# Kernel tuning notes

Hardware: AMD Instinct MI355X
Metric: run time of the kernel (lower is better)

The kernel has to match this reference:

```python
import jax, jax.numpy as jnp
import numpy as np

T, B, D = 64, 256, 2000
TN, E, H, A, V = 3000, 256, 256, 128, 128
PS, PE, S = 64, 64, 128
G1N, G1L, G2N, G2L = 1500, 4, 1500, 6


def setup_inputs():
    key = jax.random.key(0)
    ks = jax.random.split(key, 32)
    def nrm(k, shape, s=0.05):
        return jax.random.normal(k, shape, dtype=jnp.float32) * s
    inp = {}
    inp["X"] = jax.random.uniform(ks[0], (T, B, D), dtype=jnp.float32)
    inp["profiles"] = nrm(ks[1], (B, PS), 1.0)
    inp["ini_embd"] = nrm(ks[2], (TN, E), 1.0)
    inp["Wa_w"] = nrm(ks[3], (2 * E, A))
    inp["Wa_b"] = jnp.zeros((A,), jnp.float32)
    inp["Ua_w"] = nrm(ks[4], (A, 1))
    inp["gru_Wih"] = nrm(ks[5], (3 * H, E))
    inp["gru_Whh"] = nrm(ks[6], (3 * H, H))
    inp["gru_bih"] = jnp.zeros((3 * H,), jnp.float32)
    inp["gru_bhh"] = jnp.zeros((3 * H,), jnp.float32)
    inp["tranH_w"] = nrm(ks[7], (H + PE, E))
    inp["tranH_b"] = jnp.zeros((E,), jnp.float32)
    inp["out_w"] = nrm(ks[8], (H + V + PE, D))
    inp["out_b"] = jnp.zeros((D,), jnp.float32)
    inp["erase_w"] = nrm(ks[9], (E, V))
    inp["erase_b"] = jnp.zeros((V,), jnp.float32)
    inp["add_w"] = nrm(ks[10], (E, V))
    inp["add_b"] = jnp.zeros((V,), jnp.float32)
    inp["iniVam"] = nrm(ks[11], (S, V), 1.0)
    inp["emP_w"] = nrm(ks[12], (PS, PE))
    inp["emP_b"] = jnp.zeros((PE,), jnp.float32)
    inp["attnP_w"] = nrm(ks[13], (PE + V, PE))
    inp["attnP_b"] = jnp.zeros((PE,), jnp.float32)
    inp["KMIds"] = jax.random.randint(ks[14], (S,), 0, TN, dtype=jnp.int32)
    inp["leaves1"] = jax.random.randint(ks[15], (G1N, G1L), 0, TN, dtype=jnp.int32)
    inp["anc1"] = jax.random.randint(ks[16], (G1N, G1L), 0, TN, dtype=jnp.int32)
    inp["leaves2"] = jax.random.randint(ks[17], (G2N, G2L), 0, TN, dtype=jnp.int32)
    inp["anc2"] = jax.random.randint(ks[18], (G2N, G2L), 0, TN, dtype=jnp.int32)
    inp["mapInfo"] = jax.random.randint(ks[19], (D,), 0, G1N + G2N, dtype=jnp.int32)
    lens = jnp.sort(jax.random.randint(ks[20], (B,), 1, T + 1, dtype=jnp.int32))[::-1]
    inp["X_lengths"] = lens.at[0].set(T)
    return inp


def _forward(floats, ints):
    (X, profiles, ini_embd, Wa_w, Wa_b, Ua_w, gru_Wih, gru_Whh, gru_bih, gru_bhh,
     tranH_w, tranH_b, out_w, out_b, erase_w, erase_b, add_w, add_b, iniVam,
     emP_w, emP_b, attnP_w, attnP_b) = floats
    KMIds, leaves1, anc1, leaves2, anc2, mapInfo, X_lengths = ints

    # GRAM-style ontology attention over (leaf, ancestor) pairs, grouped by path length
    def group_embed(leaves, anc):
        le = ini_embd[leaves]                                     # [N,L,E]
        ae = ini_embd[anc]                                        # [N,L,E]
        hdn = jnp.tanh(jnp.concatenate([le, ae], axis=2) @ Wa_w + Wa_b)
        w = jax.nn.softmax(hdn @ Ua_w, axis=1)                    # [N,L,1]
        return jnp.sum(w * ae, axis=1)                            # [N,E]

    embedMat = jnp.concatenate([group_embed(leaves1, anc1),
                                group_embed(leaves2, anc2)], axis=0)[mapInfo]  # [D,E]
    Xe = jnp.einsum('tbd,de->tbe', X, embedMat)                   # [T,B,E]

    # packed-sequence GRU: frozen state / zero output beyond each sample's length
    mask = (jnp.arange(T)[:, None] < X_lengths[None, :])[..., None]  # [T,B,1]

    def gru_step(h, tup):
        x_t, m_t = tup
        gx = x_t @ gru_Wih.T + gru_bih
        gh = h @ gru_Whh.T + gru_bhh
        r = jax.nn.sigmoid(gx[:, :H] + gh[:, :H])
        z = jax.nn.sigmoid(gx[:, H:2 * H] + gh[:, H:2 * H])
        n = jnp.tanh(gx[:, 2 * H:] + r * gh[:, 2 * H:])
        h_new = (1.0 - z) * n + z * h
        h = jnp.where(m_t, h_new, h)
        return h, jnp.where(m_t, h, 0.0)

    h0 = jnp.zeros((B, H), jnp.float32)
    _, gru_out = jax.lax.scan(gru_step, h0, (Xe, mask))           # [T,B,H]

    prof = profiles @ emP_w + emP_b                               # [B,PE]
    prof_rep = jnp.broadcast_to(prof[None], (T, B, PE))
    tran = jnp.concatenate([gru_out, prof_rep], axis=2) @ tranH_w + tranH_b  # [T,B,E]
    KM = ini_embd[KMIds]                                          # [S,E]
    slot_w = jax.nn.softmax(jnp.einsum('tbe,se->tbs', tran, KM), axis=2)     # [T,B,S]

    # erase/add gates depend only on Xe -> precompute, then scan VM recurrence
    erase = jax.nn.sigmoid(Xe @ erase_w + erase_b)                # [T,B,V]
    add = jnp.tanh(Xe @ add_w + add_b)                            # [T,B,V]

    def mem_step(VM, tup):
        sw, er, ad = tup                                          # [B,S],[B,V],[B,V]
        read = jnp.einsum('bs,bsv->bv', sw, VM)
        VM = VM * (1.0 - sw[:, :, None] * er[:, None, :]) + sw[:, :, None] * ad[:, None, :]
        return VM, read

    VM0 = jnp.broadcast_to(iniVam[None], (B, S, V))
    _, read = jax.lax.scan(mem_step, VM0, (slot_w, erase, add))   # read: [T,B,V]

    attn = jax.nn.relu(jnp.concatenate([prof_rep, read], axis=2) @ attnP_w + attnP_b)
    prof2 = prof_rep * attn
    final = jnp.concatenate([gru_out, read, prof2], axis=2)       # [T,B,H+V+PE]
    # dropout is identity (eval / drop_rate=0)
    return jax.nn.softmax(final @ out_w + out_b, axis=2)          # [T,B,D]


def reference(X, profiles, ini_embd, Wa_w, Wa_b, Ua_w, gru_Wih, gru_Whh, gru_bih, gru_bhh, tranH_w, tranH_b, out_w, out_b, erase_w, erase_b, add_w, add_b, iniVam, emP_w, emP_b, attnP_w, attnP_b, KMIds, leaves1, anc1, leaves2, anc2, mapInfo, X_lengths):
    floats = (X, profiles, ini_embd, Wa_w, Wa_b, Ua_w, gru_Wih, gru_Whh, gru_bih, gru_bhh,
              tranH_w, tranH_b, out_w, out_b, erase_w, erase_b, add_w, add_b, iniVam,
              emP_w, emP_b, attnP_w, attnP_b)
    ints = (KMIds, leaves1, anc1, leaves2, anc2, mapInfo, X_lengths)
    return _forward(floats, ints)
```

## Files before the change

### kernel.cpp

```cpp
#include <hip/hip_runtime.h>
#include <hip/hip_bf16.h>
#include <cmath>

#define T_  64
#define B_  256
#define D_  2000
#define TN_ 3000
#define E_  256
#define H_  256
#define A_  128
#define V_  128
#define PS_ 64
#define PE_ 64
#define S_  128
#define G1N_ 1500
#define G1L_ 4
#define G2N_ 1500
#define G2L_ 6
#define M_  (T_ * B_)
#define KF_ (H_ + V_ + PE_)
#define NREG 28

typedef __attribute__((ext_vector_type(8))) short short8_t;
typedef __attribute__((ext_vector_type(4))) float floatx4;
typedef _Float16 __attribute__((ext_vector_type(2))) h2_t;
typedef _Float16 __attribute__((ext_vector_type(8))) h8_t;

static __device__ __forceinline__ float sigmoidf_(float x) {
    return 1.0f / (1.0f + __expf(-x));
}

static __device__ __forceinline__ void bsplit_(float v, __hip_bfloat16& hi, __hip_bfloat16& lo) {
    hi = __float2bfloat16(v);
    lo = __float2bfloat16(v - __bfloat162float(hi));
}

static __device__ __forceinline__ float dot2_(unsigned int w, unsigned int h, float acc) {
    union { unsigned int u; h2_t h; } cw, ch;
    cw.u = w; ch.u = h;
#if __has_builtin(__builtin_amdgcn_fdot2)
    return __builtin_amdgcn_fdot2(cw.h, ch.h, acc, false);
#else
    return acc + (float)cw.h[0] * (float)ch.h[0] + (float)cw.h[1] * (float)ch.h[1];
#endif
}

template<int DT>
static __device__ __forceinline__ floatx4 mfma16_(short8_t a, short8_t b, floatx4 c) {
    if constexpr (DT == 0) {
        return __builtin_amdgcn_mfma_f32_16x16x32_bf16(a, b, c, 0, 0, 0);
    } else {
        union { short8_t s; h8_t h; } ua, ub;
        ua.s = a; ub.s = b;
        return __builtin_amdgcn_mfma_f32_16x16x32_f16(ua.h, ub.h, c, 0, 0, 0);
    }
}

template<int EPI, bool ACCUM, int OUTMODE, int NPH, int DT>
__global__ __launch_bounds__(256)
void k_mgemm3(const __hip_bfloat16* __restrict__ Ahi, const __hip_bfloat16* __restrict__ Alo,
              const __hip_bfloat16* __restrict__ Bhi, const __hip_bfloat16* __restrict__ Blo,
              const float* __restrict__ bias, float* __restrict__ Cf,
              __hip_bfloat16* __restrict__ Chi, __hip_bfloat16* __restrict__ Clo,
              int K, int Nreal, int nblk)
{
    __shared__ __align__(16) short As[4096];
    __shared__ __align__(16) short Bs[4096];

    const int tid  = threadIdx.x;
    const int lane = tid & 63;
    const int w    = tid >> 6;
    const int wm   = w >> 1, wn = w & 1;
    const int lr   = lane & 15;
    const int lkc  = lane >> 4;

    const int bx = blockIdx.x;
    const int m0 = (bx / nblk) * 128;
    const int n0 = (bx % nblk) * 128;

    const int fa = 2 * w;
    const size_t aoff0 = (size_t)(m0 + fa * 16 + lr) * K + lkc * 8;
    const size_t aoff1 = aoff0 + (size_t)16 * K;
    const size_t boff0 = (size_t)(n0 + fa * 16 + lr) * K + lkc * 8;
    const size_t boff1 = boff0 + (size_t)16 * K;

    floatx4 acc[4][4];
#pragma unroll
    for (int i = 0; i < 4; ++i)
#pragma unroll
        for (int j = 0; j < 4; ++j) acc[i][j] = floatx4{0.f, 0.f, 0.f, 0.f};

#pragma unroll 1
    for (int ph = 0; ph < NPH; ++ph) {
        const __hip_bfloat16* Ap = (ph == 2) ? Alo : Ahi;
        const __hip_bfloat16* Bp = (ph == 1) ? Blo : Bhi;

        short8_t ra0 = *(const short8_t*)(const void*)(Ap + aoff0);
        short8_t ra1 = *(const short8_t*)(const void*)(Ap + aoff1);
        short8_t rb0 = *(const short8_t*)(const void*)(Bp + boff0);
        short8_t rb1 = *(const short8_t*)(const void*)(Bp + boff1);

        for (int k0 = 0; k0 < K; k0 += 32) {
            __syncthreads();
            *(short8_t*)(void*)&As[(fa    ) * 512 + lane * 8] = ra0;
            *(short8_t*)(void*)&As[(fa + 1) * 512 + lane * 8] = ra1;
            *(short8_t*)(void*)&Bs[(fa    ) * 512 + lane * 8] = rb0;
            *(short8_t*)(void*)&Bs[(fa + 1) * 512 + lane * 8] = rb1;
            __syncthreads();

            if (k0 + 32 < K) {
                int kn = k0 + 32;
                ra0 = *(const short8_t*)(const void*)(Ap + aoff0 + kn);
                ra1 = *(const short8_t*)(const void*)(Ap + aoff1 + kn);
                rb0 = *(const short8_t*)(const void*)(Bp + boff0 + kn);
                rb1 = *(const short8_t*)(const void*)(Bp + boff1 + kn);
            }

            short8_t af[4], bf[4];
#pragma unroll
            for (int i = 0; i < 4; ++i)
                af[i] = *(const short8_t*)(const void*)&As[(wm * 4 + i) * 512 + lane * 8];
#pragma unroll
            for (int j = 0; j < 4; ++j)
                bf[j] = *(const short8_t*)(const void*)&Bs[(wn * 4 + j) * 512 + lane * 8];
#pragma unroll
            for (int i = 0; i < 4; ++i)
#pragma unroll
                for (int j = 0; j < 4; ++j)
                    acc[i][j] = mfma16_<DT>(af[i], bf[j], acc[i][j]);
        }
    }

#pragma unroll
    for (int i = 0; i < 4; ++i) {
        const int row = m0 + wm * 64 + i * 16 + (lane >> 4) * 4;
#pragma unroll
        for (int j = 0; j < 4; ++j) {
            const int col = n0 + wn * 64 + j * 16 + (lane & 15);
            if (col < Nreal) {
                float bv = bias ? bias[col] : 0.0f;
#pragma unroll
                for (int r = 0; r < 4; ++r) {
                    float v = acc[i][j][r] + bv;
                    if (EPI == 1) v = (col < 128) ? sigmoidf_(v) : tanhf(v);
                    size_t o = (size_t)(row + r) * Nreal + col;
                    if (OUTMODE == 0) {
                        if (ACCUM) v += Cf[o];
                        Cf[o] = v;
                    } else {
                        __hip_bfloat16 h, l;
                        bsplit_(v, h, l);
                        Chi[o] = h; Clo[o] = l;
                    }
                }
            }
        }
    }
}

__global__ __launch_bounds__(256)
void k_mgemmX(const float* __restrict__ A,
              const __hip_bfloat16* __restrict__ Bhi, const __hip_bfloat16* __restrict__ Blo,
              __hip_bfloat16* __restrict__ Chi, __hip_bfloat16* __restrict__ Clo)
{
    const int KP = 2048, KR = 2000, NN = 256, nblk = 2;
    __shared__ __align__(16) short Ah[4096];
    __shared__ __align__(16) short Al[4096];
    __shared__ __align__(16) short Bh[4096];
    __shared__ __align__(16) short Bl[4096];

    const int tid  = threadIdx.x;
    const int lane = tid & 63;
    const int w    = tid >> 6;
    const int wm   = w >> 1, wn = w & 1;
    const int lr   = lane & 15;
    const int lkc  = lane >> 4;

    const int bx = blockIdx.x;
    const int m0 = (bx / nblk) * 128;
    const int n0 = (bx % nblk) * 128;

    const int fa = 2 * w;
    const float* arow0 = A + (size_t)(m0 + fa * 16 + lr) * KR;
    const float* arow1 = arow0 + (size_t)16 * KR;
    const size_t boff0 = (size_t)(n0 + fa * 16 + lr) * KP + lkc * 8;
    const size_t boff1 = boff0 + (size_t)16 * KP;

    floatx4 acc[4][4];
#pragma unroll
    for (int i = 0; i < 4; ++i)
#pragma unroll
        for (int j = 0; j < 4; ++j) acc[i][j] = floatx4{0.f, 0.f, 0.f, 0.f};

    float a0v[8], a1v[8];
    short8_t bh0, bh1, bl0, bl1;

#define LOADA8(ROW, KB, DST)                                                  \
    if ((KB) + 7 < KR) {                                                      \
        float4 p_ = *(const float4*)((ROW) + (KB));                           \
        float4 q_ = *(const float4*)((ROW) + (KB) + 4);                       \
        DST[0]=p_.x; DST[1]=p_.y; DST[2]=p_.z; DST[3]=p_.w;                   \
        DST[4]=q_.x; DST[5]=q_.y; DST[6]=q_.z; DST[7]=q_.w;                   \
    } else {                                                                  \
        _Pragma("unroll")                                                     \
        for (int ii = 0; ii < 8; ++ii)                                        \
            DST[ii] = ((KB) + ii < KR) ? (ROW)[(KB) + ii] : 0.0f;             \
    }

    {
        const int kb = lkc * 8;
        LOADA8(arow0, kb, a0v)
        LOADA8(arow1, kb, a1v)
        bh0 = *(const short8_t*)(const void*)(Bhi + boff0);
        bh1 = *(const short8_t*)(const void*)(Bhi + boff1);
        bl0 = *(const short8_t*)(const void*)(Blo + boff0);
        bl1 = *(const short8_t*)(const void*)(Blo + boff1);
    }

    for (int k0 = 0; k0 < KP; k0 += 32) {
        __syncthreads();
        {
            short h8a[8], l8a[8], h8b[8], l8b[8];
#pragma unroll
            for (int i = 0; i < 8; ++i) {
                __hip_bfloat16 h, l;
                bsplit_(a0v[i], h, l);
                h8a[i] = *(short*)&h; l8a[i] = *(short*)&l;
                bsplit_(a1v[i], h, l);
                h8b[i] = *(short*)&h; l8b[i] = *(short*)&l;
            }
            *(short8_t*)(void*)&Ah[(fa    ) * 512 + lane * 8] = *(short8_t*)h8a;
            *(short8_t*)(void*)&Al[(fa    ) * 512 + lane * 8] = *(short8_t*)l8a;
            *(short8_t*)(void*)&Ah[(fa + 1) * 512 + lane * 8] = *(short8_t*)h8b;
            *(short8_t*)(void*)&Al[(fa + 1) * 512 + lane * 8] = *(short8_t*)l8b;
            *(short8_t*)(void*)&Bh[(fa    ) * 512 + lane * 8] = bh0;
            *(short8_t*)(void*)&Bh[(fa + 1) * 512 + lane * 8] = bh1;
            *(short8_t*)(void*)&Bl[(fa    ) * 512 + lane * 8] = bl0;
            *(short8_t*)(void*)&Bl[(fa + 1) * 512 + lane * 8] = bl1;
        }
        __syncthreads();

        if (k0 + 32 < KP) {
            const int kb = k0 + 32 + lkc * 8;
            LOADA8(arow0, kb, a0v)
            LOADA8(arow1, kb, a1v)
            bh0 = *(const short8_t*)(const void*)(Bhi + boff0 + k0 + 32);
            bh1 = *(const short8_t*)(const void*)(Bhi + boff1 + k0 + 32);
            bl0 = *(const short8_t*)(const void*)(Blo + boff0 + k0 + 32);
            bl1 = *(const short8_t*)(const void*)(Blo + boff1 + k0 + 32);
        }

        short8_t afh[4], afl[4], bfh[4], bfl[4];
#pragma unroll
        for (int i = 0; i < 4; ++i) {
            afh[i] = *(const short8_t*)(const void*)&Ah[(wm * 4 + i) * 512 + lane * 8];
            bfh[i] = *(const short8_t*)(const void*)&Bh[(wn * 4 + i) * 512 + lane * 8];
        }
#pragma unroll
        for (int i = 0; i < 4; ++i)
#pragma unroll
            for (int j = 0; j < 4; ++j)
                acc[i][j] = mfma16_<0>(afh[i], bfh[j], acc[i][j]);
#pragma unroll
        for (int j = 0; j < 4; ++j)
            bfl[j] = *(const short8_t*)(const void*)&Bl[(wn * 4 + j) * 512 + lane * 8];
#pragma unroll
        for (int i = 0; i < 4; ++i)
#pragma unroll
            for (int j = 0; j < 4; ++j)
                acc[i][j] = mfma16_<0>(afh[i], bfl[j], acc[i][j]);
#pragma unroll
        for (int i = 0; i < 4; ++i)
            afl[i] = *(const short8_t*)(const void*)&Al[(wm * 4 + i) * 512 + lane * 8];
#pragma unroll
        for (int i = 0; i < 4; ++i)
#pragma unroll
            for (int j = 0; j < 4; ++j)
                acc[i][j] = mfma16_<0>(afl[i], bfh[j], acc[i][j]);
    }
#undef LOADA8

#pragma unroll
    for (int i = 0; i < 4; ++i) {
        const int row = m0 + wm * 64 + i * 16 + (lane >> 4) * 4;
#pragma unroll
        for (int j = 0; j < 4; ++j) {
            const int col = n0 + wn * 64 + j * 16 + (lane & 15);
#pragma unroll
            for (int r = 0; r < 4; ++r) {
                float v = acc[i][j][r];
                size_t o = (size_t)(row + r) * NN + col;
                __hip_bfloat16 h, l;
                bsplit_(v, h, l);
                Chi[o] = h; Clo[o] = l;
            }
        }
    }
}

template<int BM, int BN, int BK, int TM, int TN>
__global__ __launch_bounds__(256)
void k_gemm(const float* __restrict__ A, const float* __restrict__ B,
            float* __restrict__ C, int M, int N, int K)
{
    __shared__ float As[BK][BM + 4];
    __shared__ float Bs[BK][BN + 4];
    const int tid = threadIdx.y * blockDim.x + threadIdx.x;
    const int m0 = blockIdx.y * BM;
    const int n0 = blockIdx.x * BN;
    float acc[TM][TN];
#pragma unroll
    for (int i = 0; i < TM; ++i)
#pragma unroll
        for (int j = 0; j < TN; ++j) acc[i][j] = 0.0f;
    for (int k0 = 0; k0 < K; k0 += BK) {
#pragma unroll
        for (int i = tid; i < BM * BK; i += 256) {
            int r = i / BK, c = i % BK;
            int m = m0 + r;
            As[c][r] = (m < M) ? A[(size_t)m * K + k0 + c] : 0.0f;
        }
#pragma unroll
        for (int i = tid; i < BK * BN; i += 256) {
            int r = i / BN, c = i % BN;
            Bs[r][c] = B[(size_t)(k0 + r) * N + n0 + c];
        }
        __syncthreads();
#pragma unroll
        for (int kk = 0; kk < BK; ++kk) {
            float a[TM], b[TN];
#pragma unroll
            for (int i = 0; i < TM; ++i) a[i] = As[kk][threadIdx.y * TM + i];
#pragma unroll
            for (int j = 0; j < TN; ++j) b[j] = Bs[kk][threadIdx.x * TN + j];
#pragma unroll
            for (int i = 0; i < TM; ++i)
#pragma unroll
                for (int j = 0; j < TN; ++j) acc[i][j] += a[i] * b[j];
        }
        __syncthreads();
    }
#pragma unroll
    for (int i = 0; i < TM; ++i) {
        int m = m0 + threadIdx.y * TM + i;
        if (m >= M) continue;
#pragma unroll
        for (int j = 0; j < TN; ++j)
            C[(size_t)m * N + n0 + threadIdx.x * TN + j] = acc[i][j];
    }
}

__global__ void k_pack_w2(const float* __restrict__ Wa_w, float* __restrict__ W2)
{
    int idx = blockIdx.x * blockDim.x + threadIdx.x;
    if (idx >= E_ * 2 * A_) return;
    int e = idx / (2 * A_), j = idx % (2 * A_);
    W2[idx] = (j < A_) ? Wa_w[(size_t)e * A_ + j]
                       : Wa_w[(size_t)(E_ + e) * A_ + (j - A_)];
}

__global__ void k_weaT_split(const float* __restrict__ erase_w, const float* __restrict__ add_w,
                             const float* __restrict__ erase_b, const float* __restrict__ add_b,
                             __hip_bfloat16* __restrict__ Whi, __hip_bfloat16* __restrict__ Wlo,
                             float* __restrict__ bea)
{
    int idx = blockIdx.x * blockDim.x + threadIdx.x;
    if (idx < 256 * 256) {
        int n = idx / 256, k = idx % 256;
        float v = (n < V_) ? erase_w[(size_t)k * V_ + n] : add_w[(size_t)k * V_ + (n - V_)];
        bsplit_(v, Whi[idx], Wlo[idx]);
    }
    if (idx < 2 * V_) bea[idx] = (idx < V_) ? erase_b[idx] : add_b[idx - V_];
}

__global__ void k_wih_split(const float* __restrict__ Wih,
                            __hip_bfloat16* __restrict__ hi, __hip_bfloat16* __restrict__ lo)
{
    int idx = blockIdx.x * blockDim.x + threadIdx.x;
    if (idx < 768 * 256) bsplit_(Wih[idx], hi[idx], lo[idx]);
}

__global__ void k_tranHT_split(const float* __restrict__ tranH_w,
                               __hip_bfloat16* __restrict__ hi, __hip_bfloat16* __restrict__ lo)
{
    int idx = blockIdx.x * blockDim.x + threadIdx.x;
    if (idx >= 256 * 320) return;
    int n = idx / 320, k = idx % 320;
    bsplit_(tranH_w[(size_t)k * 256 + n], hi[idx], lo[idx]);
}

__global__ void k_outWT_f16(const float* __restrict__ out_w, _Float16* __restrict__ dst)
{
    int idx = blockIdx.x * blockDim.x + threadIdx.x;
    if (idx >= 2048 * 448) return;
    int n = idx / 448, k = idx % 448;
    float v = (n < D_) ? out_w[(size_t)k * D_ + n] : 0.0f;
    dst[idx] = (_Float16)v;
}

__global__ void k_km_split(const float* __restrict__ ini_embd, const int* __restrict__ KMIds,
                           __hip_bfloat16* __restrict__ hi, __hip_bfloat16* __restrict__ lo)
{
    int idx = blockIdx.x * blockDim.x + threadIdx.x;
    if (idx >= S_ * E_) return;
    int s = idx / E_, k = idx % E_;
    bsplit_(ini_embd[(size_t)KMIds[s] * E_ + k], hi[idx], lo[idx]);
}

__global__ void k_embMT(const float* __restrict__ embG, const int* __restrict__ mapInfo,
                        __hip_bfloat16* __restrict__ hi, __hip_bfloat16* __restrict__ lo)
{
    int idx = blockIdx.x * blockDim.x + threadIdx.x;
    if (idx >= 256 * 2048) return;
    int e = idx >> 11, d = idx & 2047;
    float v = (d < D_) ? embG[(size_t)mapInfo[d] * E_ + e] : 0.0f;
    bsplit_(v, hi[idx], lo[idx]);
}

__global__ void k_wgru_pack(const float* __restrict__ Whh,
                            unsigned int* __restrict__ Wrg, unsigned int* __restrict__ Wst)
{
    int idx = blockIdx.x * blockDim.x + threadIdx.x;
    if (idx >= 768 * 128) return;
    int j = idx / 128, e2 = idx % 128;
    union { unsigned int u; h2_t h; } c;
    c.h[0] = (_Float16)Whh[(size_t)j * 256 + 2 * e2];
    c.h[1] = (_Float16)Whh[(size_t)j * 256 + 2 * e2 + 1];
    if (e2 < 4 * NREG) {
        Wrg[(size_t)e2 * 768 + j] = c.u;
    } else {
        int ee = e2 - 4 * NREG;
        Wst[((size_t)(ee >> 2) * 768 + j) * 4 + (ee & 3)] = c.u;
    }
}

__global__ void k_prof(const float* __restrict__ profiles, const float* __restrict__ emP_w,
                       const float* __restrict__ emP_b, float* __restrict__ prof)
{
    int b = blockIdx.x, j = threadIdx.x;
    float acc = emP_b[j];
    for (int k = 0; k < PS_; ++k) acc += profiles[(size_t)b * PS_ + k] * emP_w[(size_t)k * PE_ + j];
    prof[(size_t)b * PE_ + j] = acc;
}

__global__ void k_fill_tp(const float* __restrict__ prof,
                          __hip_bfloat16* __restrict__ At_hi, __hip_bfloat16* __restrict__ At_lo)
{
    int idx = blockIdx.x * blockDim.x + threadIdx.x;
    if (idx >= M_ * PE_) return;
    int m = idx >> 6, pe = idx & 63;
    float v = prof[(size_t)(m & (B_ - 1)) * PE_ + pe];
    size_t o = (size_t)m * 320 + 256 + pe;
    bsplit_(v, At_hi[o], At_lo[o]);
}

__global__ void k_group_embed(const float* __restrict__ PP, const float* __restrict__ Wa_b,
                              const float* __restrict__ Ua_w, const float* __restrict__ ini_embd,
                              const int* __restrict__ leaves1, const int* __restrict__ anc1,
                              const int* __restrict__ leaves2, const int* __restrict__ anc2,
                              float* __restrict__ embedG)
{
    int n = blockIdx.x;
    int lane = threadIdx.x;
    const int* lv; const int* ac; int L;
    if (n < G1N_) { L = G1L_; lv = leaves1 + (size_t)n * G1L_; ac = anc1 + (size_t)n * G1L_; }
    else { int n2 = n - G1N_; L = G2L_; lv = leaves2 + (size_t)n2 * G2L_; ac = anc2 + (size_t)n2 * G2L_; }

    float score[6]; int ai[6];
    for (int l = 0; l < L; ++l) {
        int li = lv[l]; int av = ac[l]; ai[l] = av;
        float s = 0.0f;
        for (int a = lane; a < A_; a += 64) {
            float hv = tanhf(PP[(size_t)li * 256 + a] + PP[(size_t)av * 256 + 128 + a] + Wa_b[a]);
            s += hv * Ua_w[a];
        }
        for (int o = 32; o; o >>= 1) s += __shfl_xor(s, o);
        score[l] = s;
    }
    float mx = -1e30f;
    for (int l = 0; l < L; ++l) mx = fmaxf(mx, score[l]);
    float w[6], sum = 0.0f;
    for (int l = 0; l < L; ++l) { w[l] = __expf(score[l] - mx); sum += w[l]; }
    float inv = 1.0f / sum;
    for (int e = lane; e < E_; e += 64) {
        float acc = 0.0f;
        for (int l = 0; l < L; ++l) acc += w[l] * inv * ini_embd[(size_t)ai[l] * E_ + e];
        embedG[(size_t)n * E_ + e] = acc;
    }
}

__global__ __launch_bounds__(768, 3)
void k_gru5(const float* __restrict__ gx, const unsigned int* __restrict__ Wrg,
            const uint4* __restrict__ Wst, const float* __restrict__ bhh,
            const int* __restrict__ X_len, float* __restrict__ gruo,
            __hip_bfloat16* __restrict__ At_hi, __hip_bfloat16* __restrict__ At_lo)
{
    const int b = blockIdx.x;
    const int tid = threadIdx.x;

    __shared__ uint4 h2S[32];
    __shared__ float ghS[768];
    __shared__ float gxnS[256];

    if (tid < 128) ((unsigned int*)h2S)[tid] = 0u;

    uint4 Wr[NREG];
#pragma unroll
    for (int c = 0; c < NREG; ++c) {
        Wr[c].x = Wrg[(size_t)(4 * c + 0) * 768 + tid];
        Wr[c].y = Wrg[(size_t)(4 * c + 1) * 768 + tid];
        Wr[c].z = Wrg[(size_t)(4 * c + 2) * 768 + tid];
        Wr[c].w = Wrg[(size_t)(4 * c + 3) * 768 + tid];
    }

    float hreg = 0.0f;
    const int len = X_len[b];
    const float bj = bhh[tid];
    __syncthreads();

    for (int t = 0; t < T_; ++t) {
        float gxv = gx[((size_t)t * B_ + b) * 768 + tid];

        float a0 = bj;
#pragma unroll
        for (int c = 0; c < 32; ++c) {
            uint4 w = (c < NREG) ? Wr[c] : Wst[(size_t)(c - NREG) * 768 + tid];
            uint4 h = h2S[c];
            a0 = dot2_(w.x, h.x, a0);
            a0 = dot2_(w.y, h.y, a0);
            a0 = dot2_(w.z, h.z, a0);
            a0 = dot2_(w.w, h.w, a0);
        }

        if (tid < 512) ghS[tid] = a0 + gxv;
        else { ghS[tid] = a0; gxnS[tid - 512] = gxv; }
        __syncthreads();

        if (tid < 256) {
            float r  = sigmoidf_(ghS[tid]);
            float z  = sigmoidf_(ghS[256 + tid]);
            float nn = tanhf(gxnS[tid] + r * ghS[512 + tid]);
            float hnew = (1.0f - z) * nn + z * hreg;
            bool msk = (t < len);
            hreg = msk ? hnew : hreg;
            float ov = msk ? hreg : 0.0f;
            size_t m = (size_t)t * B_ + b;
            gruo[m * H_ + tid] = ov;
            size_t o = m * 320 + tid;
            bsplit_(ov, At_hi[o], At_lo[o]);
            float partner = __shfl_xor(hreg, 1);
            if (!(tid & 1)) {
                union { unsigned int u; h2_t h; } p;
                p.h[0] = (_Float16)hreg;
                p.h[1] = (_Float16)partner;
                ((unsigned int*)h2S)[tid >> 1] = p.u;
            }
        }
        __syncthreads();
    }
}

__global__ __launch_bounds__(256)
void k_mem(const float* __restrict__ slotw, const float* __restrict__ era,
           const float* __restrict__ iniVam, float* __restrict__ readv)
{
    const int b = blockIdx.x;
    const int tid = threadIdx.x;
    const int v = tid & (V_ - 1);
    const int sh = tid >> 7;
    const int sbase = sh * 64;

    float VM[64];
#pragma unroll
    for (int i = 0; i < 64; ++i) VM[i] = iniVam[(size_t)(sbase + i) * V_ + v];

    __shared__ float swL[S_];
    __shared__ float eaL[2 * V_];
    __shared__ float part[V_];

    for (int t = 0; t < T_; ++t) {
        size_t m = (size_t)t * B_ + b;
        if (tid < S_) swL[tid] = slotw[m * S_ + tid];
        eaL[tid] = era[m * (2 * V_) + tid];
        __syncthreads();

        float er = eaL[v], ad = eaL[V_ + v];
        float p0 = 0.0f, p1 = 0.0f, p2 = 0.0f, p3 = 0.0f;
#pragma unroll
        for (int i = 0; i < 16; ++i) {
            float s0 = swL[sbase + 4 * i];
            float s1 = swL[sbase + 4 * i + 1];
            float s2 = swL[sbase + 4 * i + 2];
            float s3 = swL[sbase + 4 * i + 3];
            float v0 = VM[4 * i], v1 = VM[4 * i + 1], v2 = VM[4 * i + 2], v3 = VM[4 * i + 3];
            p0 += s0 * v0; p1 += s1 * v1; p2 += s2 * v2; p3 += s3 * v3;
            VM[4 * i]     = v0 * (1.0f - s0 * er) + s0 * ad;
            VM[4 * i + 1] = v1 * (1.0f - s1 * er) + s1 * ad;
            VM[4 * i + 2] = v2 * (1.0f - s2 * er) + s2 * ad;
            VM[4 * i + 3] = v3 * (1.0f - s3 * er) + s3 * ad;
        }
        float acc = (p0 + p1) + (p2 + p3);
        if (sh == 1) part[v] = acc;
        __syncthreads();
        if (sh == 0) readv[m * V_ + v] = acc + part[v];
        __syncthreads();
    }
}

__global__ __launch_bounds__(256)
void k_build_final(const float* __restrict__ gruo, const float* __restrict__ readv,
                   const float* __restrict__ prof, const float* __restrict__ attnP_w,
                   const float* __restrict__ attnP_b, _Float16* __restrict__ F)
{
    const int m = blockIdx.x;
    const int b = m & (B_ - 1);
    const int tid = threadIdx.x;
    __shared__ float rd[V_];
    __shared__ float pf[PE_];
    if (tid < V_) rd[tid] = readv[(size_t)m * V_ + tid];
    if (tid < PE_) pf[tid] = prof[(size_t)b * PE_ + tid];
    __syncthreads();

    size_t base = (size_t)m * KF_;
    F[base + tid] = (_Float16)gruo[(size_t)m * H_ + tid];
    if (tid < V_) F[base + H_ + tid] = (_Float16)rd[tid];
    if (tid < PE_) {
        float a = attnP_b[tid];
        for (int k = 0; k < PE_; ++k) a += pf[k] * attnP_w[(size_t)k * PE_ + tid];
        for (int k = 0; k < V_; ++k) a += rd[k] * attnP_w[(size_t)(PE_ + k) * PE_ + tid];
        a = fmaxf(a, 0.0f);
        F[base + H_ + V_ + tid] = (_Float16)(pf[tid] * a);
    }
}

__global__ void k_softmax128(float* __restrict__ C)
{
    const int m = blockIdx.x;
    const size_t base = (size_t)m * S_;
    const int lane = threadIdx.x;
    float a = C[base + lane], b = C[base + 64 + lane];
    float mx = fmaxf(a, b);
    for (int o = 32; o; o >>= 1) mx = fmaxf(mx, __shfl_xor(mx, o));
    float e0 = __expf(a - mx), e1 = __expf(b - mx);
    float s = e0 + e1;
    for (int o = 32; o; o >>= 1) s += __shfl_xor(s, o);
    float inv = 1.0f / s;
    C[base + lane] = e0 * inv;
    C[base + 64 + lane] = e1 * inv;
}

__global__ __launch_bounds__(256)
void k_softmax2000(float* __restrict__ C)
{
    const int m = blockIdx.x;
    const size_t base = (size_t)m * D_;
    const int tid = threadIdx.x;
    const int wid = tid >> 6, lane = tid & 63;
    __shared__ float red[4], red2[4];

    float v[8];
#pragma unroll
    for (int i = 0; i < 8; ++i) {
        int d = i * 256 + tid;
        v[i] = (d < D_) ? C[base + d] : -1e30f;
    }
    float mx = v[0];
#pragma unroll
    for (int i = 1; i < 8; ++i) mx = fmaxf(mx, v[i]);
    for (int o = 32; o; o >>= 1) mx = fmaxf(mx, __shfl_xor(mx, o));
    if (lane == 0) red[wid] = mx;
    __syncthreads();
    mx = fmaxf(fmaxf(red[0], red[1]), fmaxf(red[2], red[3]));

    float sum = 0.0f;
#pragma unroll
    for (int i = 0; i < 8; ++i) { v[i] = __expf(v[i] - mx); sum += v[i]; }
    for (int o = 32; o; o >>= 1) sum += __shfl_xor(sum, o);
    if (lane == 0) red2[wid] = sum;
    __syncthreads();
    sum = red2[0] + red2[1] + red2[2] + red2[3];
    float inv = 1.0f / sum;
#pragma unroll
    for (int i = 0; i < 8; ++i) {
        int d = i * 256 + tid;
        if (d < D_) C[base + d] = v[i] * inv;
    }
}

extern "C" void kernel_launch(void* const* d_in, const int* in_sizes, int n_in,
                              void* d_out, int out_size, void* d_ws, size_t ws_size,
                              hipStream_t stream)
{
    const float* X        = (const float*)d_in[0];
    const float* profiles = (const float*)d_in[1];
    const float* ini_embd = (const float*)d_in[2];
    const float* Wa_w     = (const float*)d_in[3];
    const float* Wa_b     = (const float*)d_in[4];
    const float* Ua_w     = (const float*)d_in[5];
    const float* gru_Wih  = (const float*)d_in[6];
    const float* gru_Whh  = (const float*)d_in[7];
    const float* gru_bih  = (const float*)d_in[8];
    const float* gru_bhh  = (const float*)d_in[9];
    const float* tranH_w  = (const float*)d_in[10];
    const float* tranH_b  = (const float*)d_in[11];
    const float* out_w    = (const float*)d_in[12];
    const float* out_b    = (const float*)d_in[13];
    const float* erase_w  = (const float*)d_in[14];
    const float* erase_b  = (const float*)d_in[15];
    const float* add_w    = (const float*)d_in[16];
    const float* add_b    = (const float*)d_in[17];
    const float* iniVam   = (const float*)d_in[18];
    const float* emP_w    = (const float*)d_in[19];
    const float* emP_b    = (const float*)d_in[20];
    const float* attnP_w  = (const float*)d_in[21];
    const float* attnP_b  = (const float*)d_in[22];
    const int* KMIds   = (const int*)d_in[23];
    const int* leaves1 = (const int*)d_in[24];
    const int* anc1    = (const int*)d_in[25];
    const int* leaves2 = (const int*)d_in[26];
    const int* anc2    = (const int*)d_in[27];
    const int* mapInfo = (const int*)d_in[28];
    const int* X_len   = (const int*)d_in[29];

    char* ws = (char*)d_ws;
    float* out = (float*)d_out;
    typedef __hip_bfloat16 bf16;

    const size_t R0 = 0;
    const size_t R1 = 67108864;
    const size_t R2 = 83886080;
    const size_t R3 = 100663296;
    size_t P = 121634816;
    const size_t EMBHI = P; P += 1048576;
    const size_t EMBLO = P; P += 1048576;
    const size_t OWF  = P; P += 1835008;
    const size_t WIHI = P; P += 393216;
    const size_t WILO = P; P += 393216;
    const size_t WEHI = P; P += 131072;
    const size_t WELO = P; P += 131072;
    const size_t THHI = P; P += 163840;
    const size_t THLO = P; P += 163840;
    const size_t KMHI = P; P += 65536;
    const size_t KMLO = P; P += 65536;
    const size_t WRG  = P; P += 344064;
    const size_t WST  = P; P += 49152;
    const size_t PROF = P; P += 65536;
    const size_t BEA  = P; P += 1024;
    const size_t W2O  = P; P += 262144;

    float* PP      = (float*)(ws + R0);
    float* embG    = (float*)(ws + R0 + 12288000);
    float* gx      = (float*)(ws + R0);
    bf16*  Xe_hi   = (bf16*)(ws + R0 + 50331648);
    bf16*  Xe_lo   = (bf16*)(ws + R0 + 58720256);
    bf16*  tran_hi = (bf16*)(ws + R0);
    bf16*  tran_lo = (bf16*)(ws + R0 + 8388608);
    _Float16* F16  = (_Float16*)(ws + R0);
    float* gruo    = (float*)(ws + R1);
    float* era     = (float*)(ws + R2);
    bf16*  At_hi   = (bf16*)(ws + R3);
    bf16*  At_lo   = (bf16*)(ws + R3 + 10485760);
    float* slotw   = (float*)(ws + R3);
    float* readv   = (float*)(ws + R3 + 10485760);
    bf16*  EMBhi = (bf16*)(ws + EMBHI); bf16* EMBlo = (bf16*)(ws + EMBLO);
    _Float16* OWf = (_Float16*)(ws + OWF);
    bf16*  WIhi = (bf16*)(ws + WIHI); bf16* WIlo = (bf16*)(ws + WILO);
    bf16*  WEhi = (bf16*)(ws + WEHI); bf16* WElo = (bf16*)(ws + WELO);
    bf16*  THhi = (bf16*)(ws + THHI); bf16* THlo = (bf16*)(ws + THLO);
    bf16*  KMhi = (bf16*)(ws + KMHI); bf16* KMlo = (bf16*)(ws + KMLO);
    unsigned int* Wrg = (unsigned int*)(ws + WRG);
    unsigned int* Wst = (unsigned int*)(ws + WST);
    float* prof = (float*)(ws + PROF);
    float* bea  = (float*)(ws + BEA);
    float* W2p  = (float*)(ws + W2O);

    k_pack_w2<<<(E_ * 2 * A_ + 255) / 256, 256, 0, stream>>>(Wa_w, W2p);
    k_weaT_split<<<(256 * 256 + 255) / 256, 256, 0, stream>>>(erase_w, add_w, erase_b, add_b, WEhi, WElo, bea);
    k_wih_split<<<(768 * 256 + 255) / 256, 256, 0, stream>>>(gru_Wih, WIhi, WIlo);
    k_tranHT_split<<<(256 * 320 + 255) / 256, 256, 0, stream>>>(tranH_w, THhi, THlo);
    k_outWT_f16<<<(2048 * 448 + 255) / 256, 256, 0, stream>>>(out_w, OWf);
    k_km_split<<<(S_ * E_ + 255) / 256, 256, 0, stream>>>(ini_embd, KMIds, KMhi, KMlo);
    k_wgru_pack<<<(768 * 128 + 255) / 256, 256, 0, stream>>>(gru_Whh, Wrg, Wst);
    k_prof<<<B_, PE_, 0, stream>>>(profiles, emP_w, emP_b, prof);

    {
        dim3 blk(16, 16);
        dim3 grid(4, (TN_ + 63) / 64);
        k_gemm<64, 64, 16, 4, 4><<<grid, blk, 0, stream>>>(ini_embd, W2p, PP, TN_, 256, E_);
    }
    k_group_embed<<<G1N_ + G2N_, 64, 0, stream>>>(PP, Wa_b, Ua_w, ini_embd,
                                                  leaves1, anc1, leaves2, anc2, embG);
    k_embMT<<<(256 * 2048) / 256, 256, 0, stream>>>(embG, mapInfo, EMBhi, EMBlo);

    k_mgemmX<<<128 * 2, 256, 0, stream>>>(X, EMBhi, EMBlo, Xe_hi, Xe_lo);

    k_mgemm3<1, false, 0, 3, 0><<<128 * 2, 256, 0, stream>>>(Xe_hi, Xe_lo, WEhi, WElo,
        bea, era, nullptr, nullptr, 256, 256, 2);

    k_mgemm3<0, false, 0, 3, 0><<<128 * 6, 256, 0, stream>>>(Xe_hi, Xe_lo, WIhi, WIlo,
        gru_bih, gx, nullptr, nullptr, 256, 768, 6);

    k_gru5<<<256, 768, 0, stream>>>(gx, Wrg, (const uint4*)Wst, gru_bhh, X_len,
                                    gruo, At_hi, At_lo);
    k_fill_tp<<<(M_ * PE_) / 256, 256, 0, stream>>>(prof, At_hi, At_lo);

    k_mgemm3<0, false, 1, 3, 0><<<128 * 2, 256, 0, stream>>>(At_hi, At_lo, THhi, THlo,
        tranH_b, nullptr, tran_hi, tran_lo, 320, 256, 2);

    k_mgemm3<0, false, 0, 3, 0><<<128 * 1, 256, 0, stream>>>(tran_hi, tran_lo, KMhi, KMlo,
        nullptr, slotw, nullptr, nullptr, 256, 128, 1);

    k_softmax128<<<M_, 64, 0, stream>>>(slotw);
    k_mem<<<B_, 256, 0, stream>>>(slotw, era, iniVam, readv);
    k_build_final<<<M_, 256, 0, stream>>>(gruo, readv, prof, attnP_w, attnP_b, F16);

    k_mgemm3<0, false, 0, 1, 1><<<128 * 16, 256, 0, stream>>>(
        (const bf16*)F16, nullptr, (const bf16*)OWf, nullptr,
        out_b, out, nullptr, nullptr, 448, 2000, 16);

    k_softmax2000<<<M_, 256, 0, stream>>>(out);
}
```

Measured before the change: 648.0 us.

## Split-K the X embedding GEMM and fuse erase/add and GRU input GEMMs

The large X×EMB GEMM (K=2048, only 256 blocks) is split into four K-chunks, giving 1024 blocks that write fp32 partials. A separate reduce kernel sums the partials and performs the bf16 hi/lo split. The erase/add projection and the GRU input projection are concatenated into one 1024-wide weight and one GEMM launch with a column-ranged epilogue, and downstream kernels read from the combined output. This trades extra partial-sum memory traffic and one more launch for better CU occupancy and fewer GEMM launches. The workspace is also rearranged so the buffers do not alias.

```diff
diff --git a/kernel.cpp b/kernel.cpp
--- a/kernel.cpp
+++ b/kernel.cpp
@@ -20,6 +20,7 @@
 #define M_  (T_ * B_)
 #define KF_ (H_ + V_ + PE_)
 #define NREG 28
+#define SK_ 4
 
 typedef __attribute__((ext_vector_type(8))) short short8_t;
 typedef __attribute__((ext_vector_type(4))) float floatx4;
@@ -143,6 +144,10 @@
                 for (int r = 0; r < 4; ++r) {
                     float v = acc[i][j][r] + bv;
                     if (EPI == 1) v = (col < 128) ? sigmoidf_(v) : tanhf(v);
+                    if (EPI == 2) {
+                        if (col < 128) v = sigmoidf_(v);
+                        else if (col < 256) v = tanhf(v);
+                    }
                     size_t o = (size_t)(row + r) * Nreal + col;
                     if (OUTMODE == 0) {
                         if (ACCUM) v += Cf[o];
@@ -161,9 +166,10 @@
 __global__ __launch_bounds__(256)
 void k_mgemmX(const float* __restrict__ A,
               const __hip_bfloat16* __restrict__ Bhi, const __hip_bfloat16* __restrict__ Blo,
-              __hip_bfloat16* __restrict__ Chi, __hip_bfloat16* __restrict__ Clo)
+              float* __restrict__ P4)
 {
     const int KP = 2048, KR = 2000, NN = 256, nblk = 2;
+    const int KC = 2048 / SK_;
     __shared__ __align__(16) short Ah[4096];
     __shared__ __align__(16) short Al[4096];
     __shared__ __align__(16) short Bh[4096];
@@ -176,9 +182,12 @@
     const int lr   = lane & 15;
     const int lkc  = lane >> 4;
 
-    const int bx = blockIdx.x;
+    const int kc = blockIdx.x >> 8;
+    const int bx = blockIdx.x & 255;
     const int m0 = (bx / nblk) * 128;
     const int n0 = (bx % nblk) * 128;
+    const int KC0 = kc * KC;
+    float* dst = P4 + (size_t)kc * (M_ * 256);
 
     const int fa = 2 * w;
     const float* arow0 = A + (size_t)(m0 + fa * 16 + lr) * KR;
@@ -208,16 +217,16 @@
     }
 
     {
-        const int kb = lkc * 8;
+        const int kb = KC0 + lkc * 8;
         LOADA8(arow0, kb, a0v)
         LOADA8(arow1, kb, a1v)
-        bh0 = *(const short8_t*)(const void*)(Bhi + boff0);
-        bh1 = *(const short8_t*)(const void*)(Bhi + boff1);
-        bl0 = *(const short8_t*)(const void*)(Blo + boff0);
-        bl1 = *(const short8_t*)(const void*)(Blo + boff1);
-    }
-
-    for (int k0 = 0; k0 < KP; k0 += 32) {
+        bh0 = *(const short8_t*)(const void*)(Bhi + boff0 + KC0);
+        bh1 = *(const short8_t*)(const void*)(Bhi + boff1 + KC0);
+        bl0 = *(const short8_t*)(const void*)(Blo + boff0 + KC0);
+        bl1 = *(const short8_t*)(const void*)(Blo + boff1 + KC0);
+    }
+
+    for (int k0 = KC0; k0 < KC0 + KC; k0 += 32) {
         __syncthreads();
         {
             short h8a[8], l8a[8], h8b[8], l8b[8];
@@ -240,7 +249,7 @@
         }
         __syncthreads();
 
-        if (k0 + 32 < KP) {
+        if (k0 + 32 < KC0 + KC) {
             const int kb = k0 + 32 + lkc * 8;
             LOADA8(arow0, kb, a0v)
             LOADA8(arow1, kb, a1v)
@@ -287,15 +296,22 @@
         for (int j = 0; j < 4; ++j) {
             const int col = n0 + wn * 64 + j * 16 + (lane & 15);
 #pragma unroll
-            for (int r = 0; r < 4; ++r) {
-                float v = acc[i][j][r];
-                size_t o = (size_t)(row + r) * NN + col;
-                __hip_bfloat16 h, l;
-                bsplit_(v, h, l);
-                Chi[o] = h; Clo[o] = l;
-            }
-        }
-    }
+            for (int r = 0; r < 4; ++r)
+                dst[(size_t)(row + r) * NN + col] = acc[i][j][r];
+        }
+    }
+}
+
+__global__ void k_reduceX(const float* __restrict__ P4,
+                          __hip_bfloat16* __restrict__ hi, __hip_bfloat16* __restrict__ lo)
+{
+    int idx = blockIdx.x * blockDim.x + threadIdx.x;
+    if (idx >= M_ * 256) return;
+    const size_t CH = (size_t)M_ * 256;
+    float v = P4[idx];
+#pragma unroll
+    for (int c = 1; c < SK_; ++c) v += P4[idx + c * CH];
+    bsplit_(v, hi[idx], lo[idx]);
 }
 
 template<int BM, int BN, int BK, int TM, int TN>
@@ -359,25 +375,26 @@
                        : Wa_w[(size_t)(E_ + e) * A_ + (j - A_)];
 }
 
-__global__ void k_weaT_split(const float* __restrict__ erase_w, const float* __restrict__ add_w,
-                             const float* __restrict__ erase_b, const float* __restrict__ add_b,
-                             __hip_bfloat16* __restrict__ Whi, __hip_bfloat16* __restrict__ Wlo,
-                             float* __restrict__ bea)
+__global__ void k_wg_split(const float* __restrict__ erase_w, const float* __restrict__ add_w,
+                           const float* __restrict__ Wih,
+                           const float* __restrict__ erase_b, const float* __restrict__ add_b,
+                           const float* __restrict__ bih,
+                           __hip_bfloat16* __restrict__ WGhi, __hip_bfloat16* __restrict__ WGlo,
+                           float* __restrict__ biasG)
 {
     int idx = blockIdx.x * blockDim.x + threadIdx.x;
-    if (idx < 256 * 256) {
-        int n = idx / 256, k = idx % 256;
-        float v = (n < V_) ? erase_w[(size_t)k * V_ + n] : add_w[(size_t)k * V_ + (n - V_)];
-        bsplit_(v, Whi[idx], Wlo[idx]);
-    }
-    if (idx < 2 * V_) bea[idx] = (idx < V_) ? erase_b[idx] : add_b[idx - V_];
-}
-
-__global__ void k_wih_split(const float* __restrict__ Wih,
-                            __hip_bfloat16* __restrict__ hi, __hip_bfloat16* __restrict__ lo)
-{
-    int idx = blockIdx.x * blockDim.x + threadIdx.x;
-    if (idx < 768 * 256) bsplit_(Wih[idx], hi[idx], lo[idx]);
+    if (idx < 1024 * 256) {
+        int n = idx >> 8, k = idx & 255;
+        float v;
+        if (n < 128)      v = erase_w[(size_t)k * V_ + n];
+        else if (n < 256) v = add_w[(size_t)k * V_ + (n - 128)];
+        else              v = Wih[(size_t)(n - 256) * 256 + k];
+        bsplit_(v, WGhi[idx], WGlo[idx]);
+    }
+    if (idx < 1024)
+        biasG[idx] = (idx < 128) ? erase_b[idx]
+                   : (idx < 256) ? add_b[idx - 128]
+                                 : bih[idx - 256];
 }
 
 __global__ void k_tranHT_split(const float* __restrict__ tranH_w,
@@ -490,7 +507,7 @@
 }
 
 __global__ __launch_bounds__(768, 3)
-void k_gru5(const float* __restrict__ gx, const unsigned int* __restrict__ Wrg,
+void k_gru5(const float* __restrict__ Cg, const unsigned int* __restrict__ Wrg,
             const uint4* __restrict__ Wst, const float* __restrict__ bhh,
             const int* __restrict__ X_len, float* __restrict__ gruo,
             __hip_bfloat16* __restrict__ At_hi, __hip_bfloat16* __restrict__ At_lo)
@@ -519,7 +536,7 @@
     __syncthreads();
 
     for (int t = 0; t < T_; ++t) {
-        float gxv = gx[((size_t)t * B_ + b) * 768 + tid];
+        float gxv = Cg[((size_t)t * B_ + b) * 1024 + 256 + tid];
 
         float a0 = bj;
 #pragma unroll
@@ -561,7 +578,7 @@
 }
 
 __global__ __launch_bounds__(256)
-void k_mem(const float* __restrict__ slotw, const float* __restrict__ era,
+void k_mem(const float* __restrict__ slotw, const float* __restrict__ Cg,
            const float* __restrict__ iniVam, float* __restrict__ readv)
 {
     const int b = blockIdx.x;
@@ -581,7 +598,7 @@
     for (int t = 0; t < T_; ++t) {
         size_t m = (size_t)t * B_ + b;
         if (tid < S_) swL[tid] = slotw[m * S_ + tid];
-        eaL[tid] = era[m * (2 * V_) + tid];
+        eaL[tid] = Cg[m * 1024 + tid];
         __syncthreads();
 
         float er = eaL[v], ad = eaL[V_ + v];
@@ -734,10 +751,8 @@
     const size_t EMBHI = P; P += 1048576;
     const size_t EMBLO = P; P += 1048576;
     const size_t OWF  = P; P += 1835008;
-    const size_t WIHI = P; P += 393216;
-    const size_t WILO = P; P += 393216;
-    const size_t WEHI = P; P += 131072;
-    const size_t WELO = P; P += 131072;
+    const size_t WGHI = P; P += 524288;
+    const size_t WGLO = P; P += 524288;
     const size_t THHI = P; P += 163840;
     const size_t THLO = P; P += 163840;
     const size_t KMHI = P; P += 65536;
@@ -745,38 +760,37 @@
     const size_t WRG  = P; P += 344064;
     const size_t WST  = P; P += 49152;
     const size_t PROF = P; P += 65536;
-    const size_t BEA  = P; P += 1024;
+    const size_t BIAS = P; P += 4096;
     const size_t W2O  = P; P += 262144;
 
     float* PP      = (float*)(ws + R0);
     float* embG    = (float*)(ws + R0 + 12288000);
-    float* gx      = (float*)(ws + R0);
-    bf16*  Xe_hi   = (bf16*)(ws + R0 + 50331648);
-    bf16*  Xe_lo   = (bf16*)(ws + R0 + 58720256);
-    bf16*  tran_hi = (bf16*)(ws + R0);
-    bf16*  tran_lo = (bf16*)(ws + R0 + 8388608);
+    float* P4      = (float*)(ws + R0);
+    float* Cg      = (float*)(ws + R0);
     _Float16* F16  = (_Float16*)(ws + R0);
     float* gruo    = (float*)(ws + R1);
-    float* era     = (float*)(ws + R2);
+    bf16*  Xe_hi   = (bf16*)(ws + R2);
+    bf16*  Xe_lo   = (bf16*)(ws + R2 + 8388608);
+    bf16*  tran_hi = (bf16*)(ws + R2);
+    bf16*  tran_lo = (bf16*)(ws + R2 + 8388608);
     bf16*  At_hi   = (bf16*)(ws + R3);
     bf16*  At_lo   = (bf16*)(ws + R3 + 10485760);
     float* slotw   = (float*)(ws + R3);
     float* readv   = (float*)(ws + R3 + 10485760);
     bf16*  EMBhi = (bf16*)(ws + EMBHI); bf16* EMBlo = (bf16*)(ws + EMBLO);
     _Float16* OWf = (_Float16*)(ws + OWF);
-    bf16*  WIhi = (bf16*)(ws + WIHI); bf16* WIlo = (bf16*)(ws + WILO);
-    bf16*  WEhi = (bf16*)(ws + WEHI); bf16* WElo = (bf16*)(ws + WELO);
+    bf16*  WGhi = (bf16*)(ws + WGHI); bf16* WGlo = (bf16*)(ws + WGLO);
     bf16*  THhi = (bf16*)(ws + THHI); bf16* THlo = (bf16*)(ws + THLO);
     bf16*  KMhi = (bf16*)(ws + KMHI); bf16* KMlo = (bf16*)(ws + KMLO);
     unsigned int* Wrg = (unsigned int*)(ws + WRG);
     unsigned int* Wst = (unsigned int*)(ws + WST);
-    float* prof = (float*)(ws + PROF);
-    float* bea  = (float*)(ws + BEA);
-    float* W2p  = (float*)(ws + W2O);
+    float* prof  = (float*)(ws + PROF);
+    float* biasG = (float*)(ws + BIAS);
+    float* W2p   = (float*)(ws + W2O);
 
     k_pack_w2<<<(E_ * 2 * A_ + 255) / 256, 256, 0, stream>>>(Wa_w, W2p);
-    k_weaT_split<<<(256 * 256 + 255) / 256, 256, 0, stream>>>(erase_w, add_w, erase_b, add_b, WEhi, WElo, bea);
-    k_wih_split<<<(768 * 256 + 255) / 256, 256, 0, stream>>>(gru_Wih, WIhi, WIlo);
+    k_wg_split<<<(1024 * 256 + 255) / 256, 256, 0, stream>>>(
+        erase_w, add_w, gru_Wih, erase_b, add_b, gru_bih, WGhi, WGlo, biasG);
     k_tranHT_split<<<(256 * 320 + 255) / 256, 256, 0, stream>>>(tranH_w, THhi, THlo);
     k_outWT_f16<<<(2048 * 448 + 255) / 256, 256, 0, stream>>>(out_w, OWf);
     k_km_split<<<(S_ * E_ + 255) / 256, 256, 0, stream>>>(ini_embd, KMIds, KMhi, KMlo);
@@ -792,15 +806,13 @@
                                                   leaves1, anc1, leaves2, anc2, embG);
     k_embMT<<<(256 * 2048) / 256, 256, 0, stream>>>(embG, mapInfo, EMBhi, EMBlo);
 
-    k_mgemmX<<<128 * 2, 256, 0, stream>>>(X, EMBhi, EMBlo, Xe_hi, Xe_lo);
-
-    k_mgemm3<1, false, 0, 3, 0><<<128 * 2, 256, 0, stream>>>(Xe_hi, Xe_lo, WEhi, WElo,
-        bea, era, nullptr, nullptr, 256, 256, 2);
-
-    k_mgemm3<0, false, 0, 3, 0><<<128 * 6, 256, 0, stream>>>(Xe_hi, Xe_lo, WIhi, WIlo,
-        gru_bih, gx, nullptr, nullptr, 256, 768, 6);
-
-    k_gru5<<<256, 768, 0, stream>>>(gx, Wrg, (const uint4*)Wst, gru_bhh, X_len,
+    k_mgemmX<<<SK_ * 256, 256, 0, stream>>>(X, EMBhi, EMBlo, P4);
+    k_reduceX<<<(M_ * 256) / 256, 256, 0, stream>>>(P4, Xe_hi, Xe_lo);
+
+    k_mgemm3<2, false, 0, 3, 0><<<128 * 8, 256, 0, stream>>>(Xe_hi, Xe_lo, WGhi, WGlo,
+        biasG, Cg, nullptr, nullptr, 256, 1024, 8);
+
+    k_gru5<<<256, 768, 0, stream>>>(Cg, Wrg, (const uint4*)Wst, gru_bhh, X_len,
                                     gruo, At_hi, At_lo);
     k_fill_tp<<<(M_ * PE_) / 256, 256, 0, stream>>>(prof, At_hi, At_lo);
 
@@ -811,7 +823,7 @@
         nullptr, slotw, nullptr, nullptr, 256, 128, 1);
 
     k_softmax128<<<M_, 64, 0, stream>>>(slotw);
-    k_mem<<<B_, 256, 0, stream>>>(slotw, era, iniVam, readv);
+    k_mem<<<B_, 256, 0, stream>>>(slotw, Cg, iniVam, readv);
     k_build_final<<<M_, 256, 0, stream>>>(gruo, readv, prof, attnP_w, attnP_b, F16);
 
     k_mgemm3<0, false, 0, 1, 1><<<128 * 16, 256, 0, stream>>>(
```

After: 666.7 us. +2.9%, slower.
